# Kernel tuning notes

Measured on AMD Instinct MI355X. Metric: run time of the kernel, lower is better.

The kernel has to match this reference:

```python
import jax, jax.numpy as jnp
import numpy as np

HID = 7168; H = 128; DQ = 1536; DKV = 512; DH = 128; DR = 64; MAXS = 4096

def _rope_tables(seq_len):
    inv_freq = 1.0 / (10000.0 ** (jnp.arange(0, DR, 2, dtype=jnp.float32) / DR))
    t = jnp.arange(seq_len, dtype=jnp.float32)
    freqs = jnp.outer(t, inv_freq)              # [S, DR/2]
    emb = jnp.concatenate([freqs, freqs], -1)   # [S, DR]
    return jnp.cos(emb), jnp.sin(emb)

def _apply_rope(x, cos, sin):
    # x: [..., S, DR]; cos/sin: [S, DR]
    d = x.shape[-1]
    x1, x2 = x[..., : d // 2], x[..., d // 2 :]
    rotated = jnp.concatenate([-x2, x1], -1)
    return (x * cos + rotated * sin).astype(x.dtype)

def setup_inputs() -> dict:
    key = jax.random.key(0)
    ks = jax.random.split(key, 16)
    s = 0.02
    inp = {
        "h":    jax.random.normal(ks[0], (1, 1024, HID), jnp.float32),
        "Wdq":  jax.random.normal(ks[1], (DQ, HID), jnp.float32) * s,
        "bdq":  jnp.zeros((DQ,), jnp.float32),
        "Wdkv": jax.random.normal(ks[2], (DKV, HID), jnp.float32) * s,
        "bdkv": jnp.zeros((DKV,), jnp.float32),
        "Wuq":  jax.random.normal(ks[3], (H * DH, DQ), jnp.float32) * s,
        "buq":  jnp.zeros((H * DH,), jnp.float32),
        "Wukv": jax.random.normal(ks[4], (H * DH * 2, DKV), jnp.float32) * s,
        "bukv": jnp.zeros((H * DH * 2,), jnp.float32),
        "Wrq":  jax.random.normal(ks[5], (H * DR, DQ), jnp.float32) * s,
        "brq":  jnp.zeros((H * DR,), jnp.float32),
        "Wrk":  jax.random.normal(ks[6], (DR, HID), jnp.float32) * s,
        "brk":  jnp.zeros((DR,), jnp.float32),
        "Wo":   jax.random.normal(ks[7], (HID, H * DH), jnp.float32) * s,
        "bo":   jnp.zeros((HID,), jnp.float32),
    }
    return inp

def reference(h, Wdq, bdq, Wdkv, bdkv, Wuq, buq, Wukv, bukv, Wrq, brq, Wrk, brk, Wo, bo):
    B, S, _ = h.shape
    c_q = h @ Wdq.T + bdq              # [B,S,DQ]
    c_kv = h @ Wdkv.T + bdkv           # [B,S,DKV]
    q_c = (c_q @ Wuq.T + buq).reshape(B, S, H, DH).transpose(0, 2, 1, 3)     # [B,H,S,DH]
    kv_c = (c_kv @ Wukv.T + bukv).reshape(B, S, H, 2 * DH).transpose(0, 2, 1, 3)
    k_c, v = kv_c[..., :DH], kv_c[..., DH:]                                  # [B,H,S,DH]
    q_r = (c_q @ Wrq.T + brq).reshape(B, S, H, DR).transpose(0, 2, 1, 3)     # [B,H,S,DR]
    k_r = (h @ Wrk.T + brk).reshape(B, S, 1, DR).transpose(0, 2, 1, 3)       # [B,1,S,DR]
    cos, sin = _rope_tables(S)
    q_r = _apply_rope(q_r, cos, sin)
    k_r = _apply_rope(k_r, cos, sin)
    q = jnp.concatenate([q_c, q_r], -1)                                      # [B,H,S,DH+DR]
    k = jnp.concatenate([k_c, jnp.broadcast_to(k_r, (B, H, S, DR))], -1)
    scale = 1.0 / jnp.sqrt(jnp.float32(DH + DR))
    scores = jnp.einsum('bhqd,bhkd->bhqk', q, k) * scale
    attn = jax.nn.softmax(scores, axis=-1)
    o = jnp.einsum('bhqk,bhkd->bhqd', attn, v)        # [B,H,S,DH]
    o = o.transpose(0, 2, 1, 3).reshape(B, S, H * DH)
    return o @ Wo.T + bo
```

## Files before the change

kernel.cpp:

```cpp
#include <hip/hip_runtime.h>
#include <hip/hip_bf16.h>

#define S_LEN 1024
#define HID 7168
#define NH 128
#define DQ 1536
#define DKV 512
#define DH 128
#define DR 64

typedef __attribute__((ext_vector_type(8))) short bf16x8;
typedef __attribute__((ext_vector_type(4))) float f32x4;
typedef __attribute__((ext_vector_type(4))) float fl4;
typedef __attribute__((ext_vector_type(4))) unsigned short us4;
typedef __attribute__((ext_vector_type(8))) unsigned short us8;
typedef __attribute__((ext_vector_type(4))) unsigned int u32x4;

static __device__ __forceinline__ unsigned short f2bf(float f) {
  union { float f; unsigned int u; } v; v.f = f;
  unsigned int u = v.u;
  return (unsigned short)((u + 0x7fffu + ((u >> 16) & 1u)) >> 16);
}
static __device__ __forceinline__ float bf2f(unsigned short u) {
  union { unsigned int u; float f; } v; v.u = ((unsigned int)u) << 16;
  return v.f;
}
static __device__ __forceinline__ unsigned int cvtpk2(float lo, float hi) {
  unsigned int r;
  asm("v_cvt_pk_bf16_f32 %0, %1, %2" : "=v"(r) : "v"(lo), "v"(hi));
  return r;
}

__global__ __launch_bounds__(256) void cvt_bf16_kernel(
    const float* __restrict__ in, unsigned short* __restrict__ out, int n8) {
  int i = blockIdx.x * 256 + threadIdx.x;
  int stride = gridDim.x * 256;
  for (; i < n8; i += stride) {
    fl4 a = ((const fl4*)in)[2 * i];
    fl4 b = ((const fl4*)in)[2 * i + 1];
    us8 u = { f2bf(a[0]), f2bf(a[1]), f2bf(a[2]), f2bf(a[3]),
              f2bf(b[0]), f2bf(b[1]), f2bf(b[2]), f2bf(b[3]) };
    ((us8*)out)[i] = u;
  }
}

__global__ __launch_bounds__(256) void cvt5_kernel(
    const float* __restrict__ h,    const float* __restrict__ wdq,
    const float* __restrict__ wdkv, const float* __restrict__ wrk,
    const float* __restrict__ wukv,
    unsigned short* __restrict__ hb, unsigned short* __restrict__ w1cat,
    unsigned short* __restrict__ wukvb)
{
  const int s0 = 917504;
  const int s1 = s0 + 1376256;
  const int s2 = s1 + 458752;
  const int s3 = s2 + 57344;
  const int s4 = s3 + 2097152;
  int i = blockIdx.x * 256 + threadIdx.x;
  int stride = gridDim.x * 256;
  for (; i < s4; i += stride) {
    const float* src;
    unsigned short* dst;
    int j;
    if (i < s0)      { src = h;    dst = hb;                              j = i; }
    else if (i < s1) { src = wdq;  dst = w1cat;                           j = i - s0; }
    else if (i < s2) { src = wdkv; dst = w1cat + (size_t)1536 * 7168;     j = i - s1; }
    else if (i < s3) { src = wrk;  dst = w1cat + (size_t)2048 * 7168;     j = i - s2; }
    else             { src = wukv; dst = wukvb;                           j = i - s3; }
    fl4 a = ((const fl4*)src)[2 * j];
    fl4 b = ((const fl4*)src)[2 * j + 1];
    us8 u = { f2bf(a[0]), f2bf(a[1]), f2bf(a[2]), f2bf(a[3]),
              f2bf(b[0]), f2bf(b[1]), f2bf(b[2]), f2bf(b[3]) };
    ((us8*)dst)[j] = u;
  }
}

__global__ __launch_bounds__(256) void setup_kernel(
    const float* __restrict__ bdq, const float* __restrict__ bdkv,
    const float* __restrict__ brk, const float* __restrict__ buq,
    const float* __restrict__ brq,
    float* __restrict__ b1cat, float* __restrict__ b2cat,
    unsigned short* __restrict__ w1pad,
    float* __restrict__ ctab, float* __restrict__ stab)
{
  int i = blockIdx.x * 256 + threadIdx.x;
  if (i < 458752) w1pad[i] = 0;
  if (i < 2176) {
    float v = (i < 1536) ? bdq[i]
            : (i < 2048) ? bdkv[i - 1536]
            : (i < 2112) ? brk[i - 2048] : 0.f;
    b1cat[i] = v;
  }
  if (i < 24576)
    b2cat[i] = (i < 16384) ? buq[i] : brq[i - 16384];
  if (i < S_LEN * 32) {
    int j = i & 31, s = i >> 5;
    float invf = expf(-0.28782313662425574f * (float)j);
    float ang = (float)s * invf;
    ctab[i] = cosf(ang);
    stab[i] = sinf(ang);
  }
}

template <int OUTMODE, int WFP32, int ROPEQ = 0>
__global__ __launch_bounds__(256) void gemm_k(
    const unsigned short* __restrict__ A, int lda,
    const unsigned short* __restrict__ Wb16,
    const float* __restrict__ Wfa, const float* __restrict__ Wfb, int nsplit,
    int ldw,
    const float* __restrict__ bias,
    void* __restrict__ Cv, int ldc, size_t zstride,
    int Ncl, int ksl, float alpha,
    const float* __restrict__ ctab = nullptr,
    const float* __restrict__ stab = nullptr)
{
  const int n0 = blockIdx.x * 128;
  if (n0 >= Ncl) return;

  __shared__ unsigned short As[128 * 64];
  __shared__ unsigned short Ws[128 * 64];
  const int t = threadIdx.x;
  const int l = t & 63, w = t >> 6;
  const int r15 = l & 15, g = l >> 4;
  const int wm = (w >> 1) * 64, wn = (w & 1) * 64;
  const int m0 = blockIdx.y * 128;
  const int kbase = blockIdx.z * ksl;
  const int srow = l >> 3;
  const int scol = (l & 7) * 8;

  f32x4 acc[4][4];
#pragma unroll
  for (int i = 0; i < 4; ++i)
#pragma unroll
    for (int j = 0; j < 4; ++j) acc[i][j] = (f32x4){0.f, 0.f, 0.f, 0.f};

  const unsigned short* Ab = A + (size_t)m0 * lda;
  const unsigned short* Wb = nullptr;
  const float* Wf = nullptr;
  if constexpr (WFP32) {
    Wf = (n0 < nsplit) ? Wfa + (size_t)n0 * ldw : Wfb + (size_t)(n0 - nsplit) * ldw;
  } else {
    Wb = Wb16 + (size_t)n0 * ldw;
  }

  fl4 wx[4], wy[4];
  auto issueW = [&](int k0) {
#pragma unroll
    for (int i = 0; i < 4; ++i) {
      int c = t + 256 * i;
      const float* src = Wf + (size_t)(c >> 3) * ldw + k0 + (c & 7) * 8;
      wx[i] = *(const fl4*)src;
      wy[i] = *(const fl4*)(src + 4);
    }
  };

  if constexpr (WFP32) issueW(kbase);
  const int kend = kbase + ksl;

  for (int k0 = kbase; k0 < kend; k0 += 64) {
    if constexpr (WFP32) {
      __builtin_amdgcn_s_barrier();
      __builtin_amdgcn_sched_barrier(0);
    } else {
      __syncthreads();
    }
#pragma unroll
    for (int i = 0; i < 4; ++i) {
      int chunk = w * 4 + i;
      int row = chunk * 8 + srow;
      __builtin_amdgcn_global_load_lds(
          (const __attribute__((address_space(1))) void*)(Ab + (size_t)row * lda + k0 + scol),
          (__attribute__((address_space(3))) void*)(As + chunk * 512), 16, 0, 0);
      if constexpr (!WFP32) {
        __builtin_amdgcn_global_load_lds(
            (const __attribute__((address_space(1))) void*)(Wb + (size_t)row * ldw + k0 + scol),
            (__attribute__((address_space(3))) void*)(Ws + chunk * 512), 16, 0, 0);
      }
    }
    if constexpr (WFP32) {
      __builtin_amdgcn_sched_barrier(0);
      asm volatile("s_waitcnt vmcnt(4)" ::: "memory");
      __builtin_amdgcn_sched_barrier(0);
#pragma unroll
      for (int i = 0; i < 4; ++i) {
        int c = t + 256 * i;
        u32x4 p = { cvtpk2(wx[i][0], wx[i][1]), cvtpk2(wx[i][2], wx[i][3]),
                    cvtpk2(wy[i][0], wy[i][1]), cvtpk2(wy[i][2], wy[i][3]) };
        ((u32x4*)Ws)[c] = p;
      }
      if (k0 + 64 < kend) {
        issueW(k0 + 64);
        __builtin_amdgcn_sched_barrier(0);
        asm volatile("s_waitcnt vmcnt(8) lgkmcnt(0)" ::: "memory");
      } else {
        asm volatile("s_waitcnt vmcnt(0) lgkmcnt(0)" ::: "memory");
      }
      __builtin_amdgcn_sched_barrier(0);
      __builtin_amdgcn_s_barrier();
    } else {
      __syncthreads();
    }
#pragma unroll
    for (int kk = 0; kk < 2; ++kk) {
      bf16x8 a[4], b[4];
#pragma unroll
      for (int mt = 0; mt < 4; ++mt)
        a[mt] = *reinterpret_cast<const bf16x8*>(&As[(wm + mt * 16 + r15) * 64 + kk * 32 + 8 * g]);
#pragma unroll
      for (int nt = 0; nt < 4; ++nt)
        b[nt] = *reinterpret_cast<const bf16x8*>(&Ws[(wn + nt * 16 + r15) * 64 + kk * 32 + 8 * g]);
#pragma unroll
      for (int mt = 0; mt < 4; ++mt)
#pragma unroll
        for (int nt = 0; nt < 4; ++nt)
          acc[mt][nt] = __builtin_amdgcn_mfma_f32_16x16x32_bf16(a[mt], b[nt], acc[mt][nt], 0, 0, 0);
    }
  }

  if constexpr (OUTMODE == 1) {
    float bv[4];
#pragma unroll
    for (int nt = 0; nt < 4; ++nt) {
      int col = n0 + wn + nt * 16 + r15;
      bv[nt] = (col < Ncl) ? bias[col] : 0.f;
    }
    bool isrope = false;
    if constexpr (ROPEQ) isrope = (n0 + wn) >= 16384;
    if (ROPEQ && isrope) {
#pragma unroll
      for (int mt = 0; mt < 4; ++mt)
#pragma unroll
        for (int r = 0; r < 4; ++r) {
          int row = m0 + wm + mt * 16 + g * 4 + r;
#pragma unroll
          for (int ntp = 0; ntp < 2; ++ntp) {
            int j = ntp * 16 + r15;
            float c = ctab[row * 32 + j];
            float s = stab[row * 32 + j];
            float x1 = acc[mt][ntp][r] + bv[ntp];
            float x2 = acc[mt][ntp + 2][r] + bv[ntp + 2];
            int col1 = n0 + wn + ntp * 16 + r15;
            ((unsigned short*)Cv)[(size_t)row * ldc + col1] =
                f2bf((x1 * c - x2 * s) * alpha);
            ((unsigned short*)Cv)[(size_t)row * ldc + col1 + 32] =
                f2bf((x2 * c + x1 * s) * alpha);
          }
        }
    } else {
#pragma unroll
      for (int mt = 0; mt < 4; ++mt)
#pragma unroll
        for (int nt = 0; nt < 4; ++nt) {
          int col = n0 + wn + nt * 16 + r15;
          if (col < Ncl) {
#pragma unroll
            for (int r = 0; r < 4; ++r) {
              int row = m0 + wm + mt * 16 + g * 4 + r;
              ((unsigned short*)Cv)[(size_t)row * ldc + col] =
                  f2bf((acc[mt][nt][r] + bv[nt]) * alpha);
            }
          }
        }
    }
  } else {
    float* Cp = (float*)Cv + blockIdx.z * zstride;
#pragma unroll
    for (int mt = 0; mt < 4; ++mt)
#pragma unroll
      for (int nt = 0; nt < 4; ++nt) {
        int col = n0 + wn + nt * 16 + r15;
        if (col < Ncl) {
#pragma unroll
          for (int r = 0; r < 4; ++r) {
            int row = m0 + wm + mt * 16 + g * 4 + r;
            Cp[(size_t)row * ldc + col] = acc[mt][nt][r];
          }
        }
      }
  }
}

#define G4_DSREAD_A(buf, mh)                                                  \
  _Pragma("unroll") for (int mf = 0; mf < 4; ++mf)                            \
  _Pragma("unroll") for (int kk = 0; kk < 2; ++kk)                            \
    af[mf][kk] = rdA(buf, mh, mf, kk);

#define G4_DSREAD_B(buf, nh, breg)                                           \
  _Pragma("unroll") for (int nf = 0; nf < 2; ++nf)                            \
  _Pragma("unroll") for (int kk = 0; kk < 2; ++kk)                            \
    breg[nf][kk] = rdB(buf, nh, nf, kk);

#define G4_MFMA(mh, nh, breg)                                                 \
  __builtin_amdgcn_s_setprio(1);                                              \
  _Pragma("unroll") for (int kk = 0; kk < 2; ++kk)                            \
  _Pragma("unroll") for (int mf = 0; mf < 4; ++mf)                            \
  _Pragma("unroll") for (int nf = 0; nf < 2; ++nf)                            \
    acc[mh][nh][mf][nf] = __builtin_amdgcn_mfma_f32_16x16x32_bf16(            \
        af[mf][kk], breg[nf][kk], acc[mh][nh][mf][nf], 0, 0, 0);              \
  __builtin_amdgcn_s_setprio(0);

#define G4_BAR_IN()                                                           \
  __builtin_amdgcn_s_barrier();                                               \
  asm volatile("s_waitcnt lgkmcnt(0)" ::: "memory");                          \
  __builtin_amdgcn_sched_barrier(0);

#define G4_BAR_OUT()                                                          \
  __builtin_amdgcn_sched_barrier(0);                                          \
  __builtin_amdgcn_s_barrier();

__global__ __launch_bounds__(512, 2) void gemm_g4_8ph(
    const unsigned short* __restrict__ A,
    const unsigned short* __restrict__ W,
    float* __restrict__ pbuf)
{
  __shared__ unsigned short S[65536];
  const int t = threadIdx.x;
  const int l = t & 63, w = t >> 6;
  const int r15 = l & 15, g = l >> 4;
  const int n0 = blockIdx.x * 256;
  const int m0 = blockIdx.y * 256;
  const int kbase = blockIdx.z * 8192;
  const int NT = 128;

  const int lp = (l & 56) | ((l ^ (l >> 3)) & 7);
  const int srow = lp >> 3;
  const int scol = (lp & 7) * 8;
  const int pr = (w >> 2) * 64;
  const int pc = (w & 3) * 32;

  f32x4 acc[2][2][4][2];
#pragma unroll
  for (int a0 = 0; a0 < 2; ++a0)
#pragma unroll
    for (int a1 = 0; a1 < 2; ++a1)
#pragma unroll
      for (int a2 = 0; a2 < 4; ++a2)
#pragma unroll
        for (int a3 = 0; a3 < 2; ++a3)
          acc[a0][a1][a2][a3] = (f32x4){0.f, 0.f, 0.f, 0.f};

  auto stage = [&](int tile, int which) {
    if (tile >= NT) return;
    const int k0 = kbase + tile * 64;
    const unsigned short* gb = (which < 2)
        ? A + (size_t)(m0 + which * 128) * 16384 + k0
        : W + (size_t)(n0 + (which - 2) * 128) * 16384 + k0;
    unsigned short* dst = S + (tile & 1) * 32768 + which * 8192;
#pragma unroll
    for (int i = 0; i < 2; ++i) {
      __builtin_amdgcn_global_load_lds(
          (const __attribute__((address_space(1))) void*)(gb + (size_t)((w * 2 + i) * 8 + srow) * 16384 + scol),
          (__attribute__((address_space(3))) void*)(dst + (w * 2 + i) * 512 + l * 8), 16, 0, 0);
    }
  };

  auto rdA = [&](int buf, int mh, int mf, int kk) -> bf16x8 {
    int row = pr + mf * 16 + r15;
    int L = row * 128 + kk * 64 + g * 16;
    L ^= ((L >> 7) & 7) << 4;
    return *(const bf16x8*)((const char*)S + buf * 65536 + mh * 16384 + L);
  };
  auto rdB = [&](int buf, int nh, int nf, int kk) -> bf16x8 {
    int row = pc + nf * 16 + r15;
    int L = row * 128 + kk * 64 + g * 16;
    L ^= ((L >> 7) & 7) << 4;
    return *(const bf16x8*)((const char*)S + buf * 65536 + (2 + nh) * 16384 + L);
  };

  bf16x8 af[4][2], bA[2][2], bB[2][2];

  stage(0, 0); stage(0, 1); stage(0, 2); stage(0, 3);
  stage(1, 0); stage(1, 2); stage(1, 3);
  __builtin_amdgcn_sched_barrier(0);
  asm volatile("s_waitcnt vmcnt(6)" ::: "memory");
  __builtin_amdgcn_sched_barrier(0);
  __builtin_amdgcn_s_barrier();

  for (int i = 0; i < 64; ++i) {
    const int tb = 2 * i;
    const bool last = (i == 63);
    G4_DSREAD_A(0, 0)
    G4_DSREAD_B(0, 0, bA)
    stage(tb + 1, 1);
    G4_BAR_IN()
    G4_MFMA(0, 0, bA)
    G4_BAR_OUT()
    G4_DSREAD_B(0, 1, bB)
    stage(tb + 2, 0);
    G4_BAR_IN()
    G4_MFMA(0, 1, bB)
    G4_BAR_OUT()
    G4_DSREAD_A(0, 1)
    stage(tb + 2, 2);
    G4_BAR_IN()
    G4_MFMA(1, 1, bB)
    G4_BAR_OUT()
    stage(tb + 2, 3);
    G4_BAR_IN()
    G4_MFMA(1, 0, bA)
    if (last) { asm volatile("s_waitcnt vmcnt(0)" ::: "memory"); }
    else      { asm volatile("s_waitcnt vmcnt(6)" ::: "memory"); }
    G4_BAR_OUT()
    G4_DSREAD_A(1, 0)
    G4_DSREAD_B(1, 0, bA)
    stage(tb + 2, 1);
    G4_BAR_IN()
    G4_MFMA(0, 0, bA)
    G4_BAR_OUT()
    G4_DSREAD_B(1, 1, bB)
    stage(tb + 3, 0);
    G4_BAR_IN()
    G4_MFMA(0, 1, bB)
    G4_BAR_OUT()
    G4_DSREAD_A(1, 1)
    stage(tb + 3, 2);
    G4_BAR_IN()
    G4_MFMA(1, 1, bB)
    G4_BAR_OUT()
    stage(tb + 3, 3);
    G4_BAR_IN()
    G4_MFMA(1, 0, bA)
    if (last) { asm volatile("s_waitcnt vmcnt(0)" ::: "memory"); }
    else      { asm volatile("s_waitcnt vmcnt(6)" ::: "memory"); }
    G4_BAR_OUT()
  }

  float* Cp = pbuf + (size_t)blockIdx.z * 1024 * 7168;
#pragma unroll
  for (int mh = 0; mh < 2; ++mh)
#pragma unroll
    for (int nh = 0; nh < 2; ++nh)
#pragma unroll
      for (int mf = 0; mf < 4; ++mf)
#pragma unroll
        for (int nf = 0; nf < 2; ++nf) {
          int col = n0 + nh * 128 + pc + nf * 16 + r15;
#pragma unroll
          for (int r = 0; r < 4; ++r) {
            int row = m0 + mh * 128 + pr + mf * 16 + g * 4 + r;
            Cp[(size_t)row * 7168 + col] = acc[mh][nh][mf][nf][r];
          }
        }
}

__global__ __launch_bounds__(256) void reduce_f32_kernel(
    const float* __restrict__ pbuf, const float* __restrict__ bias,
    float* __restrict__ out, int ldo, int rowlen4, int nz, size_t zstride, int total4)
{
  int idx = blockIdx.x * 256 + threadIdx.x;
  if (idx >= total4) return;
  int r = idx / rowlen4, c4 = idx % rowlen4;
  fl4 acc = *(const fl4*)(bias + c4 * 4);
  for (int z = 0; z < nz; ++z)
    acc += *(const fl4*)(pbuf + z * zstride + (size_t)idx * 4);
  *(fl4*)(out + (size_t)r * ldo + c4 * 4) = acc;
}

__global__ __launch_bounds__(256) void reduce_bf16_kernel(
    const float* __restrict__ pbuf, const float* __restrict__ bias,
    unsigned short* __restrict__ out, int ldo, int rowlen4, int nz, size_t zstride, int total4)
{
  int idx = blockIdx.x * 256 + threadIdx.x;
  if (idx >= total4) return;
  int r = idx / rowlen4, c4 = idx % rowlen4;
  fl4 acc = *(const fl4*)(bias + c4 * 4);
  for (int z = 0; z < nz; ++z)
    acc += *(const fl4*)(pbuf + z * zstride + (size_t)idx * 4);
  us4 u = { f2bf(acc[0]), f2bf(acc[1]), f2bf(acc[2]), f2bf(acc[3]) };
  *(us4*)(out + (size_t)r * ldo + c4 * 4) = u;
}

__global__ void rope_bf16_kernel(unsigned short* __restrict__ x, int nh, int lda, int total,
                                 const float* __restrict__ ctab,
                                 const float* __restrict__ stab) {
  int idx = blockIdx.x * 256 + threadIdx.x;
  if (idx >= total) return;
  int j = idx & 31;
  int rest = idx >> 5;
  int hh = rest % nh;
  int s = rest / nh;
  float c = ctab[s * 32 + j], sn = stab[s * 32 + j];
  size_t base = (size_t)s * lda + hh * 64;
  float x1 = bf2f(x[base + j]), x2 = bf2f(x[base + j + 32]);
  x[base + j]      = f2bf(x1 * c - x2 * sn);
  x[base + j + 32] = f2bf(x2 * c + x1 * sn);
}

__global__ __launch_bounds__(256) void vtrans_kernel(
    const unsigned short* __restrict__ kvb, unsigned short* __restrict__ vt) {
  __shared__ unsigned short tl[64][72];
  const int s0 = blockIdx.x * 64;
  const int c0 = blockIdx.y * 64;
  const int t = threadIdx.x;
  const int rr = t >> 3, cc = (t & 7) * 8;
  const int hbase = (c0 >> 7) * 256 + 128 + (c0 & 127);
#pragma unroll
  for (int i = 0; i < 2; ++i) {
    int r = rr + i * 32;
    *reinterpret_cast<bf16x8*>(&tl[r][cc]) =
        *reinterpret_cast<const bf16x8*>(kvb + (size_t)(s0 + r) * 32768 + hbase + cc);
  }
  __syncthreads();
#pragma unroll
  for (int i = 0; i < 2; ++i) {
    int vc = rr + i * 32;
    unsigned short tmp[8];
#pragma unroll
    for (int j = 0; j < 8; ++j) tmp[j] = tl[cc + j][vc];
    *reinterpret_cast<bf16x8*>(&vt[(size_t)(c0 + vc) * 1024 + s0 + cc]) =
        *reinterpret_cast<bf16x8*>(tmp);
  }
}

__global__ __launch_bounds__(512) void mla_attn_kernel(
    const unsigned short* __restrict__ qcat,
    const unsigned short* __restrict__ kvb,
    const unsigned short* __restrict__ kr,
    const unsigned short* __restrict__ vt,
    unsigned short* __restrict__ obuf)
{
  __shared__ unsigned short Klds[64][200];
  __shared__ unsigned short Vlds[128][72];
  __shared__ unsigned short Plds[8][16][72];

  const int t = threadIdx.x;
  const int l = t & 63, w = t >> 6;
  const int r15 = l & 15, g = l >> 4;
  const int bid = blockIdx.x;
  const int orig = (bid & 7) * 128 + (bid >> 3);
  const int h = orig >> 3;
  const int q0 = (orig & 7) * 128;

  bf16x8 qf[6];
  const unsigned short* qrow = qcat + (size_t)(q0 + w * 16 + r15) * 24576;
#pragma unroll
  for (int kk = 0; kk < 4; ++kk)
    qf[kk] = *reinterpret_cast<const bf16x8*>(qrow + h * 128 + kk * 32 + 8 * g);
#pragma unroll
  for (int kk = 4; kk < 6; ++kk)
    qf[kk] = *reinterpret_cast<const bf16x8*>(qrow + 16384 + h * 64 + (kk - 4) * 32 + 8 * g);

  bf16x8 kreg[3], vreg[2];
  auto loadKV = [&](int kk0) {
#pragma unroll
    for (int i = 0; i < 3; ++i) {
      int c = t + 512 * i, row = c / 24, cb = c % 24;
      const unsigned short* src = (cb < 16)
          ? kvb + (size_t)(kk0 + row) * 32768 + h * 256 + cb * 8
          : kr + (size_t)(kk0 + row) * 2112 + (cb - 16) * 8;
      kreg[i] = *reinterpret_cast<const bf16x8*>(src);
    }
#pragma unroll
    for (int i = 0; i < 2; ++i) {
      int c = t + 512 * i, d = c >> 3, kb = c & 7;
      vreg[i] = *reinterpret_cast<const bf16x8*>(vt + ((size_t)h * 128 + d) * 1024 + kk0 + kb * 8);
    }
  };

  float m_r[4], l_r[4];
  f32x4 oacc[8];
#pragma unroll
  for (int r = 0; r < 4; ++r) { m_r[r] = -1e30f; l_r[r] = 0.f; }
#pragma unroll
  for (int d = 0; d < 8; ++d) oacc[d] = (f32x4){0.f, 0.f, 0.f, 0.f};

  loadKV(0);

  for (int kt = 0; kt < 16; ++kt) {
    __syncthreads();
#pragma unroll
    for (int i = 0; i < 3; ++i) {
      int c = t + 512 * i, row = c / 24, cb = c % 24;
      *reinterpret_cast<bf16x8*>(&Klds[row][cb * 8]) = kreg[i];
    }
#pragma unroll
    for (int i = 0; i < 2; ++i) {
      int c = t + 512 * i, d = c >> 3, kb = c & 7;
      *reinterpret_cast<bf16x8*>(&Vlds[d][kb * 8]) = vreg[i];
    }
    __syncthreads();
    if (kt < 15) loadKV((kt + 1) * 64);

    f32x4 sacc[4];
#pragma unroll
    for (int nt = 0; nt < 4; ++nt) sacc[nt] = (f32x4){0.f, 0.f, 0.f, 0.f};
    __builtin_amdgcn_s_setprio(1);
#pragma unroll
    for (int nt = 0; nt < 4; ++nt)
#pragma unroll
      for (int kk = 0; kk < 6; ++kk) {
        bf16x8 b = *reinterpret_cast<const bf16x8*>(&Klds[nt * 16 + r15][kk * 32 + 8 * g]);
        sacc[nt] = __builtin_amdgcn_mfma_f32_16x16x32_bf16(qf[kk], b, sacc[nt], 0, 0, 0);
      }
    __builtin_amdgcn_s_setprio(0);

    float mx[4];
#pragma unroll
    for (int r = 0; r < 4; ++r) {
      float m = fmaxf(fmaxf(sacc[0][r], sacc[1][r]), fmaxf(sacc[2][r], sacc[3][r]));
      m = fmaxf(m, __shfl_xor(m, 1));
      m = fmaxf(m, __shfl_xor(m, 2));
      m = fmaxf(m, __shfl_xor(m, 4));
      m = fmaxf(m, __shfl_xor(m, 8));
      mx[r] = m;
    }
    float grow = fmaxf(fmaxf(mx[0] - m_r[0], mx[1] - m_r[1]),
                       fmaxf(mx[2] - m_r[2], mx[3] - m_r[3]));
    if (__any(grow > 8.0f)) {
      float sc[4];
#pragma unroll
      for (int r = 0; r < 4; ++r) {
        float mn = fmaxf(m_r[r], mx[r]);
        sc[r] = __expf(m_r[r] - mn);
        m_r[r] = mn;
        l_r[r] *= sc[r];
      }
#pragma unroll
      for (int d = 0; d < 8; ++d)
#pragma unroll
        for (int r = 0; r < 4; ++r) oacc[d][r] *= sc[r];
    }
    float rsum[4] = {0.f, 0.f, 0.f, 0.f};
#pragma unroll
    for (int nt = 0; nt < 4; ++nt)
#pragma unroll
      for (int r = 0; r < 4; ++r) {
        float p = __expf(sacc[nt][r] - m_r[r]);
        rsum[r] += p;
        Plds[w][g * 4 + r][nt * 16 + r15] = f2bf(p);
      }
#pragma unroll
    for (int r = 0; r < 4; ++r) {
      float s = rsum[r];
      s += __shfl_xor(s, 1);
      s += __shfl_xor(s, 2);
      s += __shfl_xor(s, 4);
      s += __shfl_xor(s, 8);
      l_r[r] += s;
    }

    bf16x8 pa0 = *reinterpret_cast<const bf16x8*>(&Plds[w][r15][8 * g]);
    bf16x8 pa1 = *reinterpret_cast<const bf16x8*>(&Plds[w][r15][32 + 8 * g]);
    __builtin_amdgcn_s_setprio(1);
#pragma unroll
    for (int dt = 0; dt < 8; ++dt) {
      bf16x8 v0 = *reinterpret_cast<const bf16x8*>(&Vlds[dt * 16 + r15][8 * g]);
      bf16x8 v1 = *reinterpret_cast<const bf16x8*>(&Vlds[dt * 16 + r15][32 + 8 * g]);
      oacc[dt] = __builtin_amdgcn_mfma_f32_16x16x32_bf16(pa0, v0, oacc[dt], 0, 0, 0);
      oacc[dt] = __builtin_amdgcn_mfma_f32_16x16x32_bf16(pa1, v1, oacc[dt], 0, 0, 0);
    }
    __builtin_amdgcn_s_setprio(0);
  }

#pragma unroll
  for (int dt = 0; dt < 8; ++dt)
#pragma unroll
    for (int r = 0; r < 4; ++r) {
      int row = q0 + w * 16 + g * 4 + r;
      int col = h * DH + dt * 16 + r15;
      obuf[(size_t)row * 16384 + col] = f2bf(oacc[dt][r] / l_r[r]);
    }
}

extern "C" void kernel_launch(void* const* d_in, const int* in_sizes, int n_in,
                              void* d_out, int out_size, void* d_ws, size_t ws_size,
                              hipStream_t stream) {
  const float* h    = (const float*)d_in[0];
  const float* Wdq  = (const float*)d_in[1];
  const float* bdq  = (const float*)d_in[2];
  const float* Wdkv = (const float*)d_in[3];
  const float* bdkv = (const float*)d_in[4];
  const float* Wuq  = (const float*)d_in[5];
  const float* buq  = (const float*)d_in[6];
  const float* Wukv = (const float*)d_in[7];
  const float* bukv = (const float*)d_in[8];
  const float* Wrq  = (const float*)d_in[9];
  const float* brq  = (const float*)d_in[10];
  const float* Wrk  = (const float*)d_in[11];
  const float* brk  = (const float*)d_in[12];
  const float* Wo   = (const float*)d_in[13];
  const float* bo   = (const float*)d_in[14];
  float* out = (float*)d_out;

  char* ws = (char*)d_ws;
  size_t off = 0;
  auto alloc = [&](size_t bytes) {
    char* p = ws + off;
    off += (bytes + 255) & ~(size_t)255;
    return p;
  };
  unsigned short* hb    = (unsigned short*)alloc((size_t)1024 * 7168 * 2);
  unsigned short* W1cat = (unsigned short*)alloc((size_t)2176 * 7168 * 2);
  float*          b1cat = (float*)alloc(2176 * 4);
  float*          b2cat = (float*)alloc(24576 * 4);
  unsigned short* ccat  = (unsigned short*)alloc((size_t)1024 * 2112 * 2);
  unsigned short* qcat  = (unsigned short*)alloc((size_t)1024 * 24576 * 2);
  unsigned short* kvbb  = (unsigned short*)alloc((size_t)1024 * 32768 * 2);
  unsigned short* vt    = (unsigned short*)alloc((size_t)16384 * 1024 * 2);
  unsigned short* obuf  = (unsigned short*)alloc((size_t)1024 * 16384 * 2);
  float*          ctab  = (float*)alloc((size_t)S_LEN * 32 * 4);
  float*          stab  = (float*)alloc((size_t)S_LEN * 32 * 4);
  unsigned short* Wukvb = (unsigned short*)alloc((size_t)32768 * 512 * 2);
  float* pbufG1 = (float*)qcat;
  unsigned short* Wob    = (unsigned short*)(ws + ((size_t)288 << 20));
  float*          pbufG4 = (float*)(ws + ((size_t)544 << 20));

  const float scale = 0.07216878364870323f;
  const int BIGN = 1 << 30;
  dim3 blk(256);

  cvt5_kernel<<<2048, blk, 0, stream>>>(h, Wdq, Wdkv, Wrk, Wukv, hb, W1cat, Wukvb);
  setup_kernel<<<1792, blk, 0, stream>>>(bdq, bdkv, brk, buq, brq,
                                         b1cat, b2cat, W1cat + (size_t)2112 * 7168,
                                         ctab, stab);

  gemm_k<2, 0><<<dim3(24, 8, 2), blk, 0, stream>>>(
      hb, 7168, W1cat, nullptr, nullptr, BIGN, 7168, nullptr,
      pbufG1, 2112, (size_t)1024 * 2112, 2112, 3584, 1.0f);
  reduce_bf16_kernel<<<2112, blk, 0, stream>>>(pbufG1, b1cat, ccat, 2112, 528, 2,
                                               (size_t)1024 * 2112, 1024 * 2112 / 4);
  rope_bf16_kernel<<<(1024 * 32 + 255) / 256, blk, 0, stream>>>(ccat + 2048, 1, 2112, 1024 * 32, ctab, stab);

  gemm_k<1, 1, 1><<<dim3(192, 8, 1), blk, 0, stream>>>(
      ccat, 2112, nullptr, Wuq, Wrq, 16384, 1536, b2cat,
      qcat, 24576, 0, 24576, 1536, scale, ctab, stab);

  gemm_k<1, 0><<<dim3(256, 8, 1), blk, 0, stream>>>(
      ccat + 1536, 2112, Wukvb, nullptr, nullptr, BIGN, 512, bukv,
      kvbb, 32768, 0, 32768, 512, 1.0f);
  vtrans_kernel<<<dim3(16, 256), blk, 0, stream>>>(kvbb, vt);
  mla_attn_kernel<<<dim3(1024), dim3(512), 0, stream>>>(qcat, kvbb, ccat + 2048, vt, obuf);

  cvt_bf16_kernel<<<2048, blk, 0, stream>>>(Wo, Wob, (int)((size_t)7168 * 16384 / 8));
  gemm_g4_8ph<<<dim3(28, 4, 2), dim3(512), 0, stream>>>(obuf, Wob, pbufG4);
  reduce_f32_kernel<<<7168, blk, 0, stream>>>(pbufG4, bo, out,
                                              7168, 1792, 2, (size_t)1024 * 7168, 1024 * 7168 / 4);
}
```

Measured before the change: 931.9 us.

## Fuse Wo fp32-to-bf16 conversion into output GEMM W-tile staging

Drops the separate cvt_bf16_kernel pass over the 7168x16384 fp32 Wo. The output-projection GEMM now loads fp32 W rows into registers, packs them to bf16 with v_cvt_pk_bf16_f32, and writes them into the swizzled LDS tile. The software pipeline is reworked so register-staged W loads for tile k+1 overlap the MFMAs of tile k. This removes one full read and write of Wo through memory, but each GEMM block now reads fp32 W (twice the bytes) and repeats the conversion across the M-blocks. It also adds register pressure and changes the vmcnt wait schedule.

```diff
diff --git a/kernel.cpp b/kernel.cpp
--- a/kernel.cpp
+++ b/kernel.cpp
@@ -29,19 +29,6 @@
   unsigned int r;
   asm("v_cvt_pk_bf16_f32 %0, %1, %2" : "=v"(r) : "v"(lo), "v"(hi));
   return r;
-}
-
-__global__ __launch_bounds__(256) void cvt_bf16_kernel(
-    const float* __restrict__ in, unsigned short* __restrict__ out, int n8) {
-  int i = blockIdx.x * 256 + threadIdx.x;
-  int stride = gridDim.x * 256;
-  for (; i < n8; i += stride) {
-    fl4 a = ((const fl4*)in)[2 * i];
-    fl4 b = ((const fl4*)in)[2 * i + 1];
-    us8 u = { f2bf(a[0]), f2bf(a[1]), f2bf(a[2]), f2bf(a[3]),
-              f2bf(b[0]), f2bf(b[1]), f2bf(b[2]), f2bf(b[3]) };
-    ((us8*)out)[i] = u;
-  }
 }
 
 __global__ __launch_bounds__(256) void cvt5_kernel(
@@ -285,7 +272,7 @@
   _Pragma("unroll") for (int kk = 0; kk < 2; ++kk)                            \
     af[mf][kk] = rdA(buf, mh, mf, kk);
 
-#define G4_DSREAD_B(buf, nh, breg)                                           \
+#define G4_DSREAD_B(buf, nh, breg)                                            \
   _Pragma("unroll") for (int nf = 0; nf < 2; ++nf)                            \
   _Pragma("unroll") for (int kk = 0; kk < 2; ++kk)                            \
     breg[nf][kk] = rdB(buf, nh, nf, kk);
@@ -310,7 +297,7 @@
 
 __global__ __launch_bounds__(512, 2) void gemm_g4_8ph(
     const unsigned short* __restrict__ A,
-    const unsigned short* __restrict__ W,
+    const float* __restrict__ W,
     float* __restrict__ pbuf)
 {
   __shared__ unsigned short S[65536];
@@ -328,6 +315,13 @@
   const int pr = (w >> 2) * 64;
   const int pc = (w & 3) * 32;
 
+  const int wrow = t >> 2;
+  const int wcb = (t & 3) * 16;
+  int Lw0 = wrow * 128 + wcb * 2;
+  int Lw1 = Lw0 + 16;
+  Lw0 ^= ((Lw0 >> 7) & 7) << 4;
+  Lw1 ^= ((Lw1 >> 7) & 7) << 4;
+
   f32x4 acc[2][2][4][2];
 #pragma unroll
   for (int a0 = 0; a0 < 2; ++a0)
@@ -339,19 +333,36 @@
         for (int a3 = 0; a3 < 2; ++a3)
           acc[a0][a1][a2][a3] = (f32x4){0.f, 0.f, 0.f, 0.f};
 
-  auto stage = [&](int tile, int which) {
+  auto stageA = [&](int tile, int half) {
     if (tile >= NT) return;
     const int k0 = kbase + tile * 64;
-    const unsigned short* gb = (which < 2)
-        ? A + (size_t)(m0 + which * 128) * 16384 + k0
-        : W + (size_t)(n0 + (which - 2) * 128) * 16384 + k0;
-    unsigned short* dst = S + (tile & 1) * 32768 + which * 8192;
+    const unsigned short* gb = A + (size_t)(m0 + half * 128) * 16384 + k0;
+    unsigned short* dst = S + (tile & 1) * 32768 + half * 8192;
 #pragma unroll
     for (int i = 0; i < 2; ++i) {
       __builtin_amdgcn_global_load_lds(
           (const __attribute__((address_space(1))) void*)(gb + (size_t)((w * 2 + i) * 8 + srow) * 16384 + scol),
           (__attribute__((address_space(3))) void*)(dst + (w * 2 + i) * 512 + l * 8), 16, 0, 0);
     }
+  };
+
+  fl4 ws0[4], ws1[4];
+  auto issueW = [&](fl4* dreg, int tile, int half) {
+    if (tile >= NT) return;
+    const int k0 = kbase + tile * 64;
+    const float* src = W + (size_t)(n0 + half * 128 + wrow) * 16384 + k0 + wcb;
+#pragma unroll
+    for (int q = 0; q < 4; ++q) dreg[q] = *(const fl4*)(src + q * 4);
+  };
+  auto writeW = [&](const fl4* sreg, int tile, int half) {
+    if (tile >= NT) return;
+    char* base = (char*)S + (tile & 1) * 65536 + (2 + half) * 16384;
+    u32x4 p0 = { cvtpk2(sreg[0][0], sreg[0][1]), cvtpk2(sreg[0][2], sreg[0][3]),
+                 cvtpk2(sreg[1][0], sreg[1][1]), cvtpk2(sreg[1][2], sreg[1][3]) };
+    u32x4 p1 = { cvtpk2(sreg[2][0], sreg[2][1]), cvtpk2(sreg[2][2], sreg[2][3]),
+                 cvtpk2(sreg[3][0], sreg[3][1]), cvtpk2(sreg[3][2], sreg[3][3]) };
+    *(u32x4*)(base + Lw0) = p0;
+    *(u32x4*)(base + Lw1) = p1;
   };
 
   auto rdA = [&](int buf, int mh, int mf, int kk) -> bf16x8 {
@@ -369,10 +380,15 @@
 
   bf16x8 af[4][2], bA[2][2], bB[2][2];
 
-  stage(0, 0); stage(0, 1); stage(0, 2); stage(0, 3);
-  stage(1, 0); stage(1, 2); stage(1, 3);
+  issueW(ws0, 0, 0); writeW(ws0, 0, 0);
+  issueW(ws0, 0, 1); writeW(ws0, 0, 1);
+  issueW(ws0, 1, 0); writeW(ws0, 1, 0);
+  issueW(ws0, 1, 1); writeW(ws0, 1, 1);
+  stageA(0, 0); stageA(0, 1); stageA(1, 0);
+  issueW(ws0, 2, 0);
+  issueW(ws1, 2, 1);
   __builtin_amdgcn_sched_barrier(0);
-  asm volatile("s_waitcnt vmcnt(6)" ::: "memory");
+  asm volatile("s_waitcnt vmcnt(8) lgkmcnt(0)" ::: "memory");
   __builtin_amdgcn_sched_barrier(0);
   __builtin_amdgcn_s_barrier();
 
@@ -381,47 +397,48 @@
     const bool last = (i == 63);
     G4_DSREAD_A(0, 0)
     G4_DSREAD_B(0, 0, bA)
-    stage(tb + 1, 1);
+    stageA(tb + 1, 1);
     G4_BAR_IN()
     G4_MFMA(0, 0, bA)
     G4_BAR_OUT()
     G4_DSREAD_B(0, 1, bB)
-    stage(tb + 2, 0);
+    if (last) { asm volatile("s_waitcnt vmcnt(0)" ::: "memory"); }
+    writeW(ws0, tb + 2, 0);
+    issueW(ws0, tb + 3, 0);
     G4_BAR_IN()
     G4_MFMA(0, 1, bB)
     G4_BAR_OUT()
     G4_DSREAD_A(0, 1)
-    stage(tb + 2, 2);
+    stageA(tb + 2, 0);
     G4_BAR_IN()
     G4_MFMA(1, 1, bB)
     G4_BAR_OUT()
-    stage(tb + 2, 3);
+    writeW(ws1, tb + 2, 1);
+    issueW(ws1, tb + 3, 1);
     G4_BAR_IN()
     G4_MFMA(1, 0, bA)
-    if (last) { asm volatile("s_waitcnt vmcnt(0)" ::: "memory"); }
-    else      { asm volatile("s_waitcnt vmcnt(6)" ::: "memory"); }
     G4_BAR_OUT()
     G4_DSREAD_A(1, 0)
     G4_DSREAD_B(1, 0, bA)
-    stage(tb + 2, 1);
+    stageA(tb + 2, 1);
     G4_BAR_IN()
     G4_MFMA(0, 0, bA)
     G4_BAR_OUT()
     G4_DSREAD_B(1, 1, bB)
-    stage(tb + 3, 0);
+    writeW(ws0, tb + 3, 0);
+    issueW(ws0, tb + 4, 0);
     G4_BAR_IN()
     G4_MFMA(0, 1, bB)
     G4_BAR_OUT()
     G4_DSREAD_A(1, 1)
-    stage(tb + 3, 2);
+    stageA(tb + 3, 0);
     G4_BAR_IN()
     G4_MFMA(1, 1, bB)
     G4_BAR_OUT()
-    stage(tb + 3, 3);
+    writeW(ws1, tb + 3, 1);
+    issueW(ws1, tb + 4, 1);
     G4_BAR_IN()
     G4_MFMA(1, 0, bA)
-    if (last) { asm volatile("s_waitcnt vmcnt(0)" ::: "memory"); }
-    else      { asm volatile("s_waitcnt vmcnt(6)" ::: "memory"); }
     G4_BAR_OUT()
   }
 
@@ -702,8 +719,7 @@
   float*          stab  = (float*)alloc((size_t)S_LEN * 32 * 4);
   unsigned short* Wukvb = (unsigned short*)alloc((size_t)32768 * 512 * 2);
   float* pbufG1 = (float*)qcat;
-  unsigned short* Wob    = (unsigned short*)(ws + ((size_t)288 << 20));
-  float*          pbufG4 = (float*)(ws + ((size_t)544 << 20));
+  float* pbufG4 = (float*)(ws + ((size_t)544 << 20));
 
   const float scale = 0.07216878364870323f;
   const int BIGN = 1 << 30;
@@ -731,8 +747,7 @@
   vtrans_kernel<<<dim3(16, 256), blk, 0, stream>>>(kvbb, vt);
   mla_attn_kernel<<<dim3(1024), dim3(512), 0, stream>>>(qcat, kvbb, ccat + 2048, vt, obuf);
 
-  cvt_bf16_kernel<<<2048, blk, 0, stream>>>(Wo, Wob, (int)((size_t)7168 * 16384 / 8));
-  gemm_g4_8ph<<<dim3(28, 4, 2), dim3(512), 0, stream>>>(obuf, Wob, pbufG4);
+  gemm_g4_8ph<<<dim3(28, 4, 2), dim3(512), 0, stream>>>(obuf, Wo, pbufG4);
   reduce_f32_kernel<<<7168, blk, 0, stream>>>(pbufG4, bo, out,
                                               7168, 1792, 2, (size_t)1024 * 7168, 1024 * 7168 / 4);
 }
```

New measurement: 1.374 ms. +47.4%, slower.
